# Performance work log

Hardware: AMD Instinct MI355X
Metric: run time of the kernel (lower is better)

The kernel has to match this reference:

```python
import jax, jax.numpy as jnp
import numpy as np

B, T, D, H, L = 32, 1024, 512, 512, 2
OUT = 512 * 2  # output_size is doubled in setup() (bidirectional)


def setup_inputs() -> dict:
    key = jax.random.key(0)
    ks = jax.random.split(key, 9)
    s = 1.0 / np.sqrt(H)
    return {
        "x": jax.random.normal(ks[0], (B, T, D), jnp.float32),
        "h0": jnp.zeros((L, B, H), jnp.float32),
        "c0": jnp.zeros((L, B, H), jnp.float32),
        # stacked LSTM weights, gate order (i, f, g, o) as in flax LSTMCell
        "Wi_f": jax.random.normal(ks[1], (L, D, 4 * H), jnp.float32) * s,
        "Wh_f": jax.random.normal(ks[2], (L, H, 4 * H), jnp.float32) * s,
        "b_f": jnp.zeros((L, 4 * H), jnp.float32),
        "Wi_b": jax.random.normal(ks[3], (L, D, 4 * H), jnp.float32) * s,
        "Wh_b": jax.random.normal(ks[4], (L, H, 4 * H), jnp.float32) * s,
        "b_b": jnp.zeros((L, 4 * H), jnp.float32),
        "W_out": jax.random.normal(ks[5], (2 * H, OUT), jnp.float32) * s,
        "b_out": jnp.zeros((OUT,), jnp.float32),
    }


def _lstm_layer(xs, h0, c0, Wi, Wh, b):
    # xs: [T, B, Din]; scans the sequential recurrence
    def step(carry, x_t):
        h, c = carry
        gates = x_t @ Wi + h @ Wh + b  # [B, 4H]
        i, f, g, o = jnp.split(gates, 4, axis=-1)
        c = jax.nn.sigmoid(f) * c + jax.nn.sigmoid(i) * jnp.tanh(g)
        h = jax.nn.sigmoid(o) * jnp.tanh(c)
        return (h, c), h

    _, hs = jax.lax.scan(step, (h0, c0), xs)
    return hs  # [T, B, H]


def _stack(xs, h0, c0, Wi, Wh, b):
    h = xs
    for l in range(Wi.shape[0]):  # small fixed layer loop
        h = _lstm_layer(h, h0[l], c0[l], Wi[l], Wh[l], b[l])
    return h


def reference(x, h0, c0, Wi_f, Wh_f, b_f, Wi_b, Wh_b, b_b, W_out, b_out):
    xs = jnp.swapaxes(x, 0, 1)  # [T, B, D]
    hf = _stack(xs, h0, c0, Wi_f, Wh_f, b_f)                # forward in time
    hb = _stack(xs[::-1], h0, c0, Wi_b, Wh_b, b_b)[::-1]    # backward in time
    out = jax.nn.relu(jnp.concatenate([hf, hb], axis=-1)) @ W_out + b_out
    return jnp.swapaxes(out, 0, 1)  # [B, T, 2*output_size]
```

## Files before the change

### kernel.cpp

```cpp
#include <hip/hip_runtime.h>
#include <math.h>

typedef __bf16 bf16;
typedef __bf16 bf16x8 __attribute__((ext_vector_type(8)));
typedef float f32x4 __attribute__((ext_vector_type(4)));
typedef int i32x4 __attribute__((ext_vector_type(4)));
typedef unsigned int u32;

#define TT 1024
#define BB 32
#define DD 512
#define HH 512
#define NG4 2048

#define OFF_FLAGS 0ull
#define FLAG_INTS (4u*1024u*64u)
#define OFF_ABORT ((size_t)FLAG_INTS*4ull)
#define OFF_WBT   (OFF_ABORT + 1024ull)
#define OFF_PL    (OFF_WBT + 2097152ull)
#define PL_BYTES  32768ull
#define OFF_H1    (OFF_PL + 4ull*2ull*16ull*PL_BYTES)
#define FULL_ELEM ((size_t)(TT+1)*BB*HH)

#define PLP(gg, pp, slot) (ws + OFF_PL + (((size_t)((gg)*2+(pp))*16 + (size_t)(slot))*PL_BYTES))

__device__ __forceinline__ bf16x8 load16_sc(const void* p) {
  i32x4 r;
  asm volatile("global_load_dwordx4 %0, %1, off sc0 sc1" : "=v"(r) : "v"(p) : "memory");
  return __builtin_bit_cast(bf16x8, r);
}
__device__ __forceinline__ void store_short_sc(void* p, u32 v) {
  asm volatile("global_store_short %0, %1, off sc0 sc1" :: "v"(p), "v"(v) : "memory");
}

__device__ __forceinline__ bool pollrow(int* row, int lane, int* abortf) {
  int it = 0;
  while (true) {
    int v = __hip_atomic_load(row + lane, __ATOMIC_RELAXED, __HIP_MEMORY_SCOPE_AGENT);
    if (__all(v != 0)) return true;
    __builtin_amdgcn_s_sleep(1);
    if ((++it & 1023) == 0) {
      if (it > (1 << 21)) {
        __hip_atomic_store(abortf, 1, __ATOMIC_RELAXED, __HIP_MEMORY_SCOPE_AGENT);
        return false;
      }
      if (__hip_atomic_load(abortf, __ATOMIC_RELAXED, __HIP_MEMORY_SCOPE_AGENT)) return false;
    }
  }
}

__global__ void k_setup(const float* __restrict__ h0,
                        const float* __restrict__ wout,
                        unsigned char* __restrict__ ws) {
  bf16* wbt  = (bf16*)(ws + OFF_WBT);
  int* flags = (int*)(ws + OFF_FLAGS);
  const u32 wcnt = 1024u*1024u;
  const u32 pcnt = 4u*BB*HH;
  const u32 fcnt = FLAG_INTS + 1u;
  const u32 total = wcnt + pcnt + fcnt;
  for (u32 i = blockIdx.x*blockDim.x + threadIdx.x; i < total; i += gridDim.x*blockDim.x) {
    if (i < wcnt) {
      u32 j = i >> 10, k = i & 1023u;
      wbt[(size_t)j*1024u + k] = (bf16)wout[(size_t)k*1024u + j];
    } else if (i < wcnt + pcnt) {
      u32 t = i - wcnt;
      u32 g = t >> 14;
      u32 rem = t & 16383u;
      u32 l = g >> 1;
      float v = h0[(size_t)l*(BB*HH) + rem];
      bf16 hi = (bf16)v;
      bf16 lo = (bf16)(v - (float)hi);
      ((bf16*)PLP(g, 0, 15))[rem] = hi;
      ((bf16*)PLP(g, 1, 15))[rem] = lo;
    } else {
      flags[i - wcnt - pcnt] = 0;
    }
  }
}

__launch_bounds__(256, 1)
__global__ void k_rnn(const float* __restrict__ x,
                      const float* __restrict__ c0,
                      const float* __restrict__ Wi_f, const float* __restrict__ Wh_f, const float* __restrict__ b_f,
                      const float* __restrict__ Wi_b, const float* __restrict__ Wh_b, const float* __restrict__ b_b,
                      unsigned char* __restrict__ ws) {
  __shared__ float gb[4][32][33];
  __shared__ int sab;

  const int bid = blockIdx.x;
  const int g = bid & 3;
  const int w = bid >> 2;
  const int l = g >> 1, d = g & 1;
  const int tid = threadIdx.x;
  const int lane = tid & 63;
  const int q = tid >> 6;

  const float* Wi   = (d ? Wi_b : Wi_f) + (size_t)l*DD*NG4;
  const float* Wh   = (d ? Wh_b : Wh_f) + (size_t)l*HH*NG4;
  const float* bias = (d ? b_b : b_f) + (size_t)l*NG4;

  int* flags  = (int*)(ws + OFF_FLAGS);
  int* abortf = flags + FLAG_INTS;

  const int lrow = lane & 15;
  const int kr0  = (lane >> 4) * 8;

  bf16x8 BWi[4][2], BWh[4][2], BWlo[4][2];
#pragma unroll
  for (int j = 0; j < 4; ++j) {
    int k0 = (q*4 + j)*32 + kr0;
#pragma unroll
    for (int nt = 0; nt < 2; ++nt) {
      int cc = nt*16 + lrow;
      int unit = cc >> 2, gate = cc & 3;
      int Jcol = gate*512 + w*8 + unit;
      bf16x8 ai, ah, al;
#pragma unroll
      for (int e = 0; e < 8; ++e) {
        float wi = Wi[(size_t)(k0+e)*NG4 + Jcol];
        float wh = Wh[(size_t)(k0+e)*NG4 + Jcol];
        ai[e] = (bf16)wi;
        bf16 hh = (bf16)wh;
        ah[e] = hh;
        al[e] = (bf16)(wh - (float)hh);
      }
      BWi[j][nt] = ai; BWh[j][nt] = ah; BWlo[j][nt] = al;
    }
  }

  u32 aoff[4][2];
#pragma unroll
  for (int j = 0; j < 4; ++j)
#pragma unroll
    for (int mt = 0; mt < 2; ++mt)
      aoff[j][mt] = (u32)((((mt*16 + lrow)*512) + (q*4 + j)*32 + kr0) * 2);

  const int bthr = tid >> 3, uthr = tid & 7;
  const int hu = w*8 + uthr;
  float cst = c0[((size_t)l*BB + bthr)*HH + hu];
  const float bgi = bias[hu], bgf = bias[512+hu], bgg = bias[1024+hu], bgo = bias[1536+hu];

  if (tid == 0) sab = 0;
  __syncthreads();

  for (int s = 0; s < TT; ++s) {
    const int slot_w = s & 15;
    const int slot_r = (s + 15) & 15;

    if (l == 1) {
      if (q == 1) { if (!pollrow(flags + ((size_t)d*1024 + s)*64, lane, abortf)) sab = 1; }
      __syncthreads();
    }

    f32x4 acc[2][2];
#pragma unroll
    for (int mt = 0; mt < 2; ++mt)
#pragma unroll
      for (int nt = 0; nt < 2; ++nt) acc[mt][nt] = (f32x4){0.f,0.f,0.f,0.f};

    if (l == 0) {
      const int t_time = d ? (TT-1-s) : s;
      bf16x8 Ax[4][2];
#pragma unroll
      for (int j = 0; j < 4; ++j)
#pragma unroll
        for (int mt = 0; mt < 2; ++mt) {
          const float* px = x + ((size_t)(mt*16 + lrow)*TT + t_time)*DD + (q*4 + j)*32 + kr0;
          float4 a  = *(const float4*)px;
          float4 b4 = *(const float4*)(px + 4);
          bf16x8 v = { (bf16)a.x,(bf16)a.y,(bf16)a.z,(bf16)a.w,
                       (bf16)b4.x,(bf16)b4.y,(bf16)b4.z,(bf16)b4.w };
          Ax[j][mt] = v;
        }
      if (q == 0 && s > 0)   { if (!pollrow(flags + ((size_t)g*1024 + (s-1))*64, lane, abortf)) sab = 1; }
      if (q == 1 && s >= 16) { if (!pollrow(flags + ((size_t)(2+d)*1024 + (s-16))*64, lane, abortf)) sab = 1; }
#pragma unroll
      for (int j = 0; j < 4; ++j)
#pragma unroll
        for (int mt = 0; mt < 2; ++mt)
#pragma unroll
          for (int nt = 0; nt < 2; ++nt)
            acc[mt][nt] = __builtin_amdgcn_mfma_f32_16x16x32_bf16(Ax[j][mt], BWi[j][nt], acc[mt][nt], 0, 0, 0);
    } else {
      const unsigned char* xb = PLP(d, 0, slot_w);
      bf16x8 Ax[4][2];
#pragma unroll
      for (int j = 0; j < 4; ++j)
#pragma unroll
        for (int mt = 0; mt < 2; ++mt)
          Ax[j][mt] = load16_sc(xb + aoff[j][mt]);
      if (q == 0 && s > 0) { if (!pollrow(flags + ((size_t)g*1024 + (s-1))*64, lane, abortf)) sab = 1; }
      asm volatile("s_waitcnt vmcnt(0)" ::: "memory");
      __builtin_amdgcn_sched_barrier(0);
#pragma unroll
      for (int j = 0; j < 4; ++j)
#pragma unroll
        for (int mt = 0; mt < 2; ++mt)
#pragma unroll
          for (int nt = 0; nt < 2; ++nt)
            acc[mt][nt] = __builtin_amdgcn_mfma_f32_16x16x32_bf16(Ax[j][mt], BWi[j][nt], acc[mt][nt], 0, 0, 0);
    }
    __syncthreads();
    if (sab) return;

    const unsigned char* hb = PLP(g, 0, slot_r);
    const unsigned char* lb = PLP(g, 1, slot_r);
    bf16x8 Ahi[4][2], Alo[4][2];
#pragma unroll
    for (int j = 0; j < 4; ++j)
#pragma unroll
      for (int mt = 0; mt < 2; ++mt) {
        Ahi[j][mt] = load16_sc(hb + aoff[j][mt]);
        Alo[j][mt] = load16_sc(lb + aoff[j][mt]);
      }
    asm volatile("s_waitcnt vmcnt(0)" ::: "memory");
    __builtin_amdgcn_sched_barrier(0);
#pragma unroll
    for (int j = 0; j < 4; ++j) {
#pragma unroll
      for (int mt = 0; mt < 2; ++mt)
#pragma unroll
        for (int nt = 0; nt < 2; ++nt)
          acc[mt][nt] = __builtin_amdgcn_mfma_f32_16x16x32_bf16(Ahi[j][mt], BWh[j][nt], acc[mt][nt], 0, 0, 0);
#pragma unroll
      for (int mt = 0; mt < 2; ++mt)
#pragma unroll
        for (int nt = 0; nt < 2; ++nt)
          acc[mt][nt] = __builtin_amdgcn_mfma_f32_16x16x32_bf16(Alo[j][mt], BWh[j][nt], acc[mt][nt], 0, 0, 0);
#pragma unroll
      for (int mt = 0; mt < 2; ++mt)
#pragma unroll
        for (int nt = 0; nt < 2; ++nt)
          acc[mt][nt] = __builtin_amdgcn_mfma_f32_16x16x32_bf16(Ahi[j][mt], BWlo[j][nt], acc[mt][nt], 0, 0, 0);
    }

#pragma unroll
    for (int mt = 0; mt < 2; ++mt)
#pragma unroll
      for (int nt = 0; nt < 2; ++nt)
#pragma unroll
        for (int r = 0; r < 4; ++r)
          gb[q][mt*16 + (lane>>4)*4 + r][nt*16 + lrow] = acc[mt][nt][r];
    __syncthreads();

    float gi = bgi, gf = bgf, gg2 = bgg, go = bgo;
#pragma unroll
    for (int qq = 0; qq < 4; ++qq) {
      gi  += gb[qq][bthr][uthr*4 + 0];
      gf  += gb[qq][bthr][uthr*4 + 1];
      gg2 += gb[qq][bthr][uthr*4 + 2];
      go  += gb[qq][bthr][uthr*4 + 3];
    }
    float si = 1.f/(1.f + __expf(-gi));
    float sf = 1.f/(1.f + __expf(-gf));
    float so = 1.f/(1.f + __expf(-go));
    cst = sf*cst + si*tanhf(gg2);
    float h = so*tanhf(cst);

    bf16 hh = (bf16)h;
    bf16 hl = (bf16)(h - (float)hh);
    u32 off2 = (u32)((bthr*512 + hu) * 2);
    store_short_sc((void*)(PLP(g, 0, slot_w) + off2), (u32)__builtin_bit_cast(unsigned short, hh));
    store_short_sc((void*)(PLP(g, 1, slot_w) + off2), (u32)__builtin_bit_cast(unsigned short, hl));
    if (l == 1) {
      float* H1 = (float*)(ws + OFF_H1) + (size_t)d*FULL_ELEM;
      H1[((size_t)(s+1)*BB + bthr)*HH + hu] = h;
    }
    asm volatile("s_waitcnt vmcnt(0)" ::: "memory");
    __syncthreads();
    if (tid == 0)
      __hip_atomic_store(flags + ((size_t)g*1024 + s)*64 + w, 1,
                         __ATOMIC_RELAXED, __HIP_MEMORY_SCOPE_AGENT);
  }
}

#define SWZG(row, bc) ((u32)(row)*128u + ((u32)(bc) ^ ((((u32)(row))&7u)<<4)))

__launch_bounds__(256, 2)
__global__ void k_out(const unsigned char* __restrict__ ws,
                      const float* __restrict__ bout,
                      float* __restrict__ out) {
  __shared__ unsigned char As[64*128];
  __shared__ unsigned char Bs[128*128];
  const float* Hf = (const float*)(ws + OFF_H1);
  const float* Hb = Hf + FULL_ELEM;
  const bf16* wbt = (const bf16*)(ws + OFF_WBT);

  const int m0 = blockIdx.x * 64;
  const int j0 = blockIdx.y * 128;
  const int tid = threadIdx.x, lane = tid & 63, q = tid >> 6;
  const int b = m0 >> 10;
  const int t0 = m0 & 1023;

  f32x4 acc[2][4];
#pragma unroll
  for (int mi = 0; mi < 2; ++mi)
#pragma unroll
    for (int ni = 0; ni < 4; ++ni) acc[mi][ni] = (f32x4){0.f,0.f,0.f,0.f};

  for (int kb = 0; kb < 16; ++kb) {
#pragma unroll
    for (int it = 0; it < 2; ++it) {
      int row = tid >> 2;
      int chunk = (tid & 3) + it*4;
      int k0 = kb*64 + chunk*8;
      int t = t0 + row;
      const float* src = (k0 < 512)
        ? (Hf + ((size_t)(t+1)*BB + b)*HH + k0)
        : (Hb + ((size_t)(TT-t)*BB + b)*HH + (k0-512));
      float4 fa = *(const float4*)src;
      float4 fb = *(const float4*)(src + 4);
      bf16x8 v = { (bf16)fmaxf(fa.x,0.f),(bf16)fmaxf(fa.y,0.f),(bf16)fmaxf(fa.z,0.f),(bf16)fmaxf(fa.w,0.f),
                   (bf16)fmaxf(fb.x,0.f),(bf16)fmaxf(fb.y,0.f),(bf16)fmaxf(fb.z,0.f),(bf16)fmaxf(fb.w,0.f) };
      *(bf16x8*)(As + SWZG(row, chunk*16)) = v;
    }
#pragma unroll
    for (int it = 0; it < 4; ++it) {
      int j = (tid >> 3) + it*32;
      int chunk = tid & 7;
      int k0 = kb*64 + chunk*8;
      bf16x8 v = *(const bf16x8*)(wbt + (size_t)(j0+j)*1024 + k0);
      *(bf16x8*)(Bs + SWZG(j, chunk*16)) = v;
    }
    __syncthreads();
    const int mrow = (q & 1)*32;
    const int nc0 = (q >> 1)*64;
#pragma unroll
    for (int ks = 0; ks < 2; ++ks) {
      u32 koff = (u32)(ks*32 + (lane>>4)*8) * 2u;
      bf16x8 afr[2];
#pragma unroll
      for (int mi = 0; mi < 2; ++mi)
        afr[mi] = *(const bf16x8*)(As + SWZG(mrow + mi*16 + (lane&15), koff));
#pragma unroll
      for (int ni = 0; ni < 4; ++ni) {
        bf16x8 bfr = *(const bf16x8*)(Bs + SWZG(nc0 + ni*16 + (lane&15), koff));
#pragma unroll
        for (int mi = 0; mi < 2; ++mi)
          acc[mi][ni] = __builtin_amdgcn_mfma_f32_16x16x32_bf16(afr[mi], bfr, acc[mi][ni], 0, 0, 0);
      }
    }
    __syncthreads();
  }
#pragma unroll
  for (int ni = 0; ni < 4; ++ni) {
    int col = j0 + (q >> 1)*64 + ni*16 + (lane & 15);
    float bv = bout[col];
#pragma unroll
    for (int mi = 0; mi < 2; ++mi) {
#pragma unroll
      for (int r = 0; r < 4; ++r) {
        int m = m0 + (q & 1)*32 + mi*16 + (lane >> 4)*4 + r;
        out[(size_t)m*1024 + col] = acc[mi][ni][r] + bv;
      }
    }
  }
}

extern "C" void kernel_launch(void* const* d_in, const int* in_sizes, int n_in,
                              void* d_out, int out_size, void* d_ws, size_t ws_size,
                              hipStream_t stream) {
  const float* x    = (const float*)d_in[0];
  const float* h0   = (const float*)d_in[1];
  const float* c0   = (const float*)d_in[2];
  const float* Wi_f = (const float*)d_in[3];
  const float* Wh_f = (const float*)d_in[4];
  const float* b_f  = (const float*)d_in[5];
  const float* Wi_b = (const float*)d_in[6];
  const float* Wh_b = (const float*)d_in[7];
  const float* b_b  = (const float*)d_in[8];
  const float* Wo   = (const float*)d_in[9];
  const float* bo   = (const float*)d_in[10];
  unsigned char* ws = (unsigned char*)d_ws;
  float* out = (float*)d_out;

  hipLaunchKernelGGL(k_setup, dim3(256), dim3(256), 0, stream, h0, Wo, ws);

  void* args[] = { (void*)&x, (void*)&c0, (void*)&Wi_f, (void*)&Wh_f, (void*)&b_f,
                   (void*)&Wi_b, (void*)&Wh_b, (void*)&b_b, (void*)&ws };
  hipError_t e = hipLaunchCooperativeKernel((const void*)k_rnn, dim3(256), dim3(256),
                                            args, 0, stream);
  if (e != hipSuccess) {
    hipLaunchKernelGGL(k_rnn, dim3(256), dim3(256), 0, stream,
                       x, c0, Wi_f, Wh_f, b_f, Wi_b, Wh_b, b_b, ws);
  }

  hipLaunchKernelGGL(k_out, dim3(512, 8), dim3(256), 0, stream,
                     (const unsigned char*)ws, bo, out);
}
```

Before: 6.435 ms.

## Prepack LSTM weight fragments, interleave hi/lo hidden state, prefetch x, store bf16 H1

The setup kernel now pre-packs the Wi/Wh hi/lo bf16 MFMA fragments, so each persistent RNN block loads them with contiguous 16-byte reads instead of strided scalar fp32 loads. The hi and lo bf16 halves of the hidden state are interleaved into one 32-bit word, so one store and paired vector loads replace two separate planes. Layer 0 prefetches the next timestep's x into registers while the current step runs. Polling spins briefly before sleeping and adds an acquire load. Layer-1 outputs are stored as bf16, halving output-GEMM input traffic at a small precision cost, and per-step unpacking adds ALU work.

```diff
diff --git a/kernel.cpp b/kernel.cpp
--- a/kernel.cpp
+++ b/kernel.cpp
@@ -6,86 +6,113 @@
 typedef float f32x4 __attribute__((ext_vector_type(4)));
 typedef int i32x4 __attribute__((ext_vector_type(4)));
 typedef unsigned int u32;
+typedef unsigned short u16;
 
 #define TT 1024
 #define BB 32
-#define DD 512
 #define HH 512
-#define NG4 2048
 
 #define OFF_FLAGS 0ull
-#define FLAG_INTS (4u*1024u*64u)
-#define OFF_ABORT ((size_t)FLAG_INTS*4ull)
-#define OFF_WBT   (OFF_ABORT + 1024ull)
-#define OFF_PL    (OFF_WBT + 2097152ull)
-#define PL_BYTES  32768ull
-#define OFF_H1    (OFF_PL + 4ull*2ull*16ull*PL_BYTES)
-#define FULL_ELEM ((size_t)(TT+1)*BB*HH)
-
-#define PLP(gg, pp, slot) (ws + OFF_PL + (((size_t)((gg)*2+(pp))*16 + (size_t)(slot))*PL_BYTES))
-
-__device__ __forceinline__ bf16x8 load16_sc(const void* p) {
-  i32x4 r;
-  asm volatile("global_load_dwordx4 %0, %1, off sc0 sc1" : "=v"(r) : "v"(p) : "memory");
-  return __builtin_bit_cast(bf16x8, r);
+#define OFF_CTL   1048576ull
+#define OFF_WBT   (OFF_CTL + 1024ull)
+#define OFF_FRAG  (OFF_WBT + 2097152ull)
+#define FRAG_B    8388608ull
+#define OFF_PL    (OFF_FRAG + 3ull*FRAG_B)
+#define PL_SLOT   65536ull
+#define PL_GRP    (16ull*PL_SLOT)
+#define OFF_H1    (OFF_PL + 4ull*PL_GRP)
+#define H1_ELEM   ((size_t)(TT+1)*BB*HH)
+
+__global__ void k_setup(const float* __restrict__ h0, const float* __restrict__ wout,
+                        const float* __restrict__ Wi_f, const float* __restrict__ Wh_f,
+                        const float* __restrict__ Wi_b, const float* __restrict__ Wh_b,
+                        unsigned char* __restrict__ ws) {
+  const u32 N0 = 1048576;
+  const u32 N1 = 65536;
+  const u32 N3 = 2097152;
+  const u32 N4 = 2097152;
+  const u32 N5 = 262145;
+  const u32 total = N0 + N1 + N3 + N4 + N5;
+  for (u32 i = blockIdx.x*blockDim.x + threadIdx.x; i < total; i += gridDim.x*blockDim.x) {
+    if (i < N0) {
+      u32 jj = i >> 10, kk = i & 1023u;
+      ((bf16*)(ws + OFF_WBT))[(size_t)jj*1024 + kk] = (bf16)wout[(size_t)kk*1024 + jj];
+    } else if (i < N0 + N1) {
+      u32 t = i - N0;
+      u32 g = t >> 14, r = t & 16383u;
+      u32 b = r >> 9, u = r & 511u, l = g >> 1;
+      float v = h0[((size_t)l*BB + b)*HH + u];
+      bf16 hi = (bf16)v;
+      bf16 lo = (bf16)(v - (float)hi);
+      u32 word = (u32)__builtin_bit_cast(u16, hi) | ((u32)__builtin_bit_cast(u16, lo) << 16);
+      *(u32*)(ws + OFF_PL + (size_t)g*PL_GRP + 15ull*PL_SLOT + (size_t)r*4) = word;
+    } else if (i < N0 + N1 + N3 + N4) {
+      u32 t = i - N0 - N1;
+      int isWh = (t >= N3);
+      if (isWh) t -= N3;
+      u32 e2 = t & 3u, lane = (t>>2)&63u, nt = (t>>8)&1u, j = (t>>9)&3u;
+      u32 q = (t>>11)&3u, w2 = (t>>13)&63u, g = (t>>19)&3u;
+      u32 l = g >> 1, d = g & 1;
+      u32 lrow = lane & 15u, kr0 = (lane>>4)*8u;
+      u32 cc = nt*16 + lrow;
+      u32 unit = cc >> 2, gate = cc & 3u;
+      u32 J = gate*512 + w2*8 + unit;
+      u32 k = (q*4 + j)*32 + kr0 + e2*2;
+      const float* src = isWh ? ((d ? Wh_b : Wh_f) + (size_t)l*HH*2048)
+                              : ((d ? Wi_b : Wi_f) + (size_t)l*HH*2048);
+      float v0 = src[(size_t)k*2048 + J];
+      float v1 = src[(size_t)(k+1)*2048 + J];
+      size_t fo = ((((size_t)(g*64+w2)*4 + q)*4 + j)*2 + nt)*64 + lane;
+      size_t byte = fo*16 + e2*4;
+      if (!isWh) {
+        *(u32*)(ws + OFF_FRAG + byte) =
+          (u32)__builtin_bit_cast(u16,(bf16)v0) | ((u32)__builtin_bit_cast(u16,(bf16)v1) << 16);
+      } else {
+        bf16 h0b = (bf16)v0, h1b = (bf16)v1;
+        bf16 l0b = (bf16)(v0 - (float)h0b), l1b = (bf16)(v1 - (float)h1b);
+        *(u32*)(ws + OFF_FRAG + FRAG_B + byte) =
+          (u32)__builtin_bit_cast(u16,h0b) | ((u32)__builtin_bit_cast(u16,h1b) << 16);
+        *(u32*)(ws + OFF_FRAG + 2ull*FRAG_B + byte) =
+          (u32)__builtin_bit_cast(u16,l0b) | ((u32)__builtin_bit_cast(u16,l1b) << 16);
+      }
+    } else {
+      u32 t = i - (N0+N1+N3+N4);
+      if (t < 262144u) ((int*)(ws + OFF_FLAGS))[t] = 0;
+      else *(int*)(ws + OFF_CTL) = 0;
+    }
+  }
 }
-__device__ __forceinline__ void store_short_sc(void* p, u32 v) {
-  asm volatile("global_store_short %0, %1, off sc0 sc1" :: "v"(p), "v"(v) : "memory");
-}
-
-__device__ __forceinline__ bool pollrow(int* row, int lane, int* abortf) {
+
+#define LD16(dst, p) asm volatile("global_load_dwordx4 %0, %1, off sc0 sc1" : "=v"(dst) : "v"(p) : "memory")
+#define ST4(p, v)    asm volatile("global_store_dword %0, %1, off sc0 sc1" :: "v"(p), "v"(v) : "memory")
+#define WAIT0() do { asm volatile("s_waitcnt vmcnt(0)" ::: "memory"); __builtin_amdgcn_sched_barrier(0); } while (0)
+
+__device__ __forceinline__ bool pollrow64(int* row, int lane, int* abortf) {
   int it = 0;
   while (true) {
     int v = __hip_atomic_load(row + lane, __ATOMIC_RELAXED, __HIP_MEMORY_SCOPE_AGENT);
-    if (__all(v != 0)) return true;
-    __builtin_amdgcn_s_sleep(1);
-    if ((++it & 1023) == 0) {
-      if (it > (1 << 21)) {
+    if (__all(v != 0)) {
+      (void)__hip_atomic_load(row + lane, __ATOMIC_ACQUIRE, __HIP_MEMORY_SCOPE_AGENT);
+      return true;
+    }
+    ++it;
+    if (it > 32) __builtin_amdgcn_s_sleep(1);
+    if ((it & 255) == 0) {
+      if (__hip_atomic_load(abortf, __ATOMIC_RELAXED, __HIP_MEMORY_SCOPE_AGENT)) return false;
+      if (it > (1 << 20)) {
         __hip_atomic_store(abortf, 1, __ATOMIC_RELAXED, __HIP_MEMORY_SCOPE_AGENT);
         return false;
       }
-      if (__hip_atomic_load(abortf, __ATOMIC_RELAXED, __HIP_MEMORY_SCOPE_AGENT)) return false;
     }
   }
 }
 
-__global__ void k_setup(const float* __restrict__ h0,
-                        const float* __restrict__ wout,
-                        unsigned char* __restrict__ ws) {
-  bf16* wbt  = (bf16*)(ws + OFF_WBT);
-  int* flags = (int*)(ws + OFF_FLAGS);
-  const u32 wcnt = 1024u*1024u;
-  const u32 pcnt = 4u*BB*HH;
-  const u32 fcnt = FLAG_INTS + 1u;
-  const u32 total = wcnt + pcnt + fcnt;
-  for (u32 i = blockIdx.x*blockDim.x + threadIdx.x; i < total; i += gridDim.x*blockDim.x) {
-    if (i < wcnt) {
-      u32 j = i >> 10, k = i & 1023u;
-      wbt[(size_t)j*1024u + k] = (bf16)wout[(size_t)k*1024u + j];
-    } else if (i < wcnt + pcnt) {
-      u32 t = i - wcnt;
-      u32 g = t >> 14;
-      u32 rem = t & 16383u;
-      u32 l = g >> 1;
-      float v = h0[(size_t)l*(BB*HH) + rem];
-      bf16 hi = (bf16)v;
-      bf16 lo = (bf16)(v - (float)hi);
-      ((bf16*)PLP(g, 0, 15))[rem] = hi;
-      ((bf16*)PLP(g, 1, 15))[rem] = lo;
-    } else {
-      flags[i - wcnt - pcnt] = 0;
-    }
-  }
-}
-
 __launch_bounds__(256, 1)
-__global__ void k_rnn(const float* __restrict__ x,
-                      const float* __restrict__ c0,
-                      const float* __restrict__ Wi_f, const float* __restrict__ Wh_f, const float* __restrict__ b_f,
-                      const float* __restrict__ Wi_b, const float* __restrict__ Wh_b, const float* __restrict__ b_b,
+__global__ void k_rnn(const float* __restrict__ x, const float* __restrict__ c0,
+                      const float* __restrict__ b_f, const float* __restrict__ b_b,
                       unsigned char* __restrict__ ws) {
   __shared__ float gb[4][32][33];
-  __shared__ int sab;
+  __shared__ int sdead;
 
   const int bid = blockIdx.x;
   const int g = bid & 3;
@@ -94,61 +121,61 @@
   const int tid = threadIdx.x;
   const int lane = tid & 63;
   const int q = tid >> 6;
-
-  const float* Wi   = (d ? Wi_b : Wi_f) + (size_t)l*DD*NG4;
-  const float* Wh   = (d ? Wh_b : Wh_f) + (size_t)l*HH*NG4;
-  const float* bias = (d ? b_b : b_f) + (size_t)l*NG4;
-
-  int* flags  = (int*)(ws + OFF_FLAGS);
-  int* abortf = flags + FLAG_INTS;
-
   const int lrow = lane & 15;
-  const int kr0  = (lane >> 4) * 8;
+  const int kr0 = (lane >> 4) * 8;
+
+  int* abortf = (int*)(ws + OFF_CTL);
+  int* flagw  = (int*)(ws + OFF_FLAGS);
+
+  if (tid == 0) sdead = 0;
 
   bf16x8 BWi[4][2], BWh[4][2], BWlo[4][2];
 #pragma unroll
-  for (int j = 0; j < 4; ++j) {
-    int k0 = (q*4 + j)*32 + kr0;
+  for (int j = 0; j < 4; ++j)
 #pragma unroll
     for (int nt = 0; nt < 2; ++nt) {
-      int cc = nt*16 + lrow;
-      int unit = cc >> 2, gate = cc & 3;
-      int Jcol = gate*512 + w*8 + unit;
-      bf16x8 ai, ah, al;
-#pragma unroll
-      for (int e = 0; e < 8; ++e) {
-        float wi = Wi[(size_t)(k0+e)*NG4 + Jcol];
-        float wh = Wh[(size_t)(k0+e)*NG4 + Jcol];
-        ai[e] = (bf16)wi;
-        bf16 hh = (bf16)wh;
-        ah[e] = hh;
-        al[e] = (bf16)(wh - (float)hh);
-      }
-      BWi[j][nt] = ai; BWh[j][nt] = ah; BWlo[j][nt] = al;
-    }
-  }
-
-  u32 aoff[4][2];
-#pragma unroll
-  for (int j = 0; j < 4; ++j)
-#pragma unroll
-    for (int mt = 0; mt < 2; ++mt)
-      aoff[j][mt] = (u32)((((mt*16 + lrow)*512) + (q*4 + j)*32 + kr0) * 2);
+      size_t fo = (((((size_t)(g*64+w)*4 + q)*4 + j)*2 + nt)*64 + lane) * 16;
+      BWi[j][nt]  = *(const bf16x8*)(ws + OFF_FRAG + fo);
+      BWh[j][nt]  = *(const bf16x8*)(ws + OFF_FRAG + FRAG_B + fo);
+      BWlo[j][nt] = *(const bf16x8*)(ws + OFF_FRAG + 2ull*FRAG_B + fo);
+    }
 
   const int bthr = tid >> 3, uthr = tid & 7;
   const int hu = w*8 + uthr;
   float cst = c0[((size_t)l*BB + bthr)*HH + hu];
+  const float* bias = (d ? b_b : b_f) + (size_t)l*2048;
   const float bgi = bias[hu], bgf = bias[512+hu], bgg = bias[1024+hu], bgo = bias[1536+hu];
 
-  if (tid == 0) sab = 0;
+  unsigned char* plOwn = ws + OFF_PL + (size_t)g*PL_GRP;
+  const unsigned char* plIn = ws + OFF_PL + (size_t)d*PL_GRP;
+  bf16* H1p = (bf16*)(ws + OFF_H1) + (size_t)d*H1_ELEM;
+
+  u32 ao[4][2];
+#pragma unroll
+  for (int j = 0; j < 4; ++j)
+#pragma unroll
+    for (int mt = 0; mt < 2; ++mt)
+      ao[j][mt] = (u32)((((mt*16 + lrow)*512) + (q*4 + j)*32 + kr0) * 4);
+
   __syncthreads();
+
+  float4 xr[16];
+  if (l == 0) {
+    int t0i = d ? (TT-1) : 0;
+#pragma unroll
+    for (int f = 0; f < 8; ++f) {
+      int j = f >> 1, mt = f & 1;
+      const float* px = x + (((size_t)(mt*16+lrow))*TT + t0i)*512 + (q*4 + j)*32 + kr0;
+      xr[f*2]   = *(const float4*)px;
+      xr[f*2+1] = *(const float4*)(px + 4);
+    }
+  }
 
   for (int s = 0; s < TT; ++s) {
     const int slot_w = s & 15;
-    const int slot_r = (s + 15) & 15;
 
     if (l == 1) {
-      if (q == 1) { if (!pollrow(flags + ((size_t)d*1024 + s)*64, lane, abortf)) sab = 1; }
+      if (q == 1) { if (!pollrow64(flagw + (size_t)(d*1024 + s)*64, lane, abortf)) sdead = 1; }
       __syncthreads();
     }
 
@@ -159,80 +186,92 @@
       for (int nt = 0; nt < 2; ++nt) acc[mt][nt] = (f32x4){0.f,0.f,0.f,0.f};
 
     if (l == 0) {
-      const int t_time = d ? (TT-1-s) : s;
-      bf16x8 Ax[4][2];
+      if (q == 0 && s > 0)  { if (!pollrow64(flagw + (size_t)(g*1024 + s-1)*64, lane, abortf)) sdead = 1; }
+      if (q == 1 && s >= 16){ if (!pollrow64(flagw + (size_t)((2+d)*1024 + s-16)*64, lane, abortf)) sdead = 1; }
+#pragma unroll
+      for (int f = 0; f < 8; ++f) {
+        int j = f >> 1, mt = f & 1;
+        float4 a = xr[f*2], b4 = xr[f*2+1];
+        bf16x8 ax = { (bf16)a.x,(bf16)a.y,(bf16)a.z,(bf16)a.w,
+                      (bf16)b4.x,(bf16)b4.y,(bf16)b4.z,(bf16)b4.w };
+#pragma unroll
+        for (int nt = 0; nt < 2; ++nt)
+          acc[mt][nt] = __builtin_amdgcn_mfma_f32_16x16x32_bf16(ax, BWi[j][nt], acc[mt][nt], 0, 0, 0);
+      }
+      if (s + 1 < TT) {
+        int tn = d ? (TT-2-s) : (s+1);
+#pragma unroll
+        for (int f = 0; f < 8; ++f) {
+          int j = f >> 1, mt = f & 1;
+          const float* px = x + (((size_t)(mt*16+lrow))*TT + tn)*512 + (q*4 + j)*32 + kr0;
+          xr[f*2]   = *(const float4*)px;
+          xr[f*2+1] = *(const float4*)(px + 4);
+        }
+      }
+    } else {
+      const unsigned char* xs = plIn + (size_t)slot_w*PL_SLOT;
+      i32x4 xm[4][2][2];
 #pragma unroll
       for (int j = 0; j < 4; ++j)
 #pragma unroll
         for (int mt = 0; mt < 2; ++mt) {
-          const float* px = x + ((size_t)(mt*16 + lrow)*TT + t_time)*DD + (q*4 + j)*32 + kr0;
-          float4 a  = *(const float4*)px;
-          float4 b4 = *(const float4*)(px + 4);
-          bf16x8 v = { (bf16)a.x,(bf16)a.y,(bf16)a.z,(bf16)a.w,
-                       (bf16)b4.x,(bf16)b4.y,(bf16)b4.z,(bf16)b4.w };
-          Ax[j][mt] = v;
+          LD16(xm[j][mt][0], xs + ao[j][mt]);
+          LD16(xm[j][mt][1], xs + ao[j][mt] + 16);
         }
-      if (q == 0 && s > 0)   { if (!pollrow(flags + ((size_t)g*1024 + (s-1))*64, lane, abortf)) sab = 1; }
-      if (q == 1 && s >= 16) { if (!pollrow(flags + ((size_t)(2+d)*1024 + (s-16))*64, lane, abortf)) sab = 1; }
+      if (q == 0 && s > 0) { if (!pollrow64(flagw + (size_t)(g*1024 + s-1)*64, lane, abortf)) sdead = 1; }
+      WAIT0();
 #pragma unroll
       for (int j = 0; j < 4; ++j)
 #pragma unroll
-        for (int mt = 0; mt < 2; ++mt)
+        for (int mt = 0; mt < 2; ++mt) {
+          i32x4 w0 = xm[j][mt][0], w1 = xm[j][mt][1];
+          i32x4 hi4;
+          hi4[0] = (int)(((u32)w0[0] & 0xFFFFu) | ((u32)w0[1] << 16));
+          hi4[1] = (int)(((u32)w0[2] & 0xFFFFu) | ((u32)w0[3] << 16));
+          hi4[2] = (int)(((u32)w1[0] & 0xFFFFu) | ((u32)w1[1] << 16));
+          hi4[3] = (int)(((u32)w1[2] & 0xFFFFu) | ((u32)w1[3] << 16));
+          bf16x8 ax = __builtin_bit_cast(bf16x8, hi4);
 #pragma unroll
           for (int nt = 0; nt < 2; ++nt)
-            acc[mt][nt] = __builtin_amdgcn_mfma_f32_16x16x32_bf16(Ax[j][mt], BWi[j][nt], acc[mt][nt], 0, 0, 0);
-    } else {
-      const unsigned char* xb = PLP(d, 0, slot_w);
-      bf16x8 Ax[4][2];
-#pragma unroll
-      for (int j = 0; j < 4; ++j)
-#pragma unroll
-        for (int mt = 0; mt < 2; ++mt)
-          Ax[j][mt] = load16_sc(xb + aoff[j][mt]);
-      if (q == 0 && s > 0) { if (!pollrow(flags + ((size_t)g*1024 + (s-1))*64, lane, abortf)) sab = 1; }
-      asm volatile("s_waitcnt vmcnt(0)" ::: "memory");
-      __builtin_amdgcn_sched_barrier(0);
-#pragma unroll
-      for (int j = 0; j < 4; ++j)
-#pragma unroll
-        for (int mt = 0; mt < 2; ++mt)
-#pragma unroll
-          for (int nt = 0; nt < 2; ++nt)
-            acc[mt][nt] = __builtin_amdgcn_mfma_f32_16x16x32_bf16(Ax[j][mt], BWi[j][nt], acc[mt][nt], 0, 0, 0);
+            acc[mt][nt] = __builtin_amdgcn_mfma_f32_16x16x32_bf16(ax, BWi[j][nt], acc[mt][nt], 0, 0, 0);
+        }
     }
     __syncthreads();
-    if (sab) return;
-
-    const unsigned char* hb = PLP(g, 0, slot_r);
-    const unsigned char* lb = PLP(g, 1, slot_r);
-    bf16x8 Ahi[4][2], Alo[4][2];
+    if (sdead) return;
+
+    const unsigned char* hs = plOwn + (size_t)((s + 15) & 15)*PL_SLOT;
+    i32x4 hw[4][2][2];
 #pragma unroll
     for (int j = 0; j < 4; ++j)
 #pragma unroll
       for (int mt = 0; mt < 2; ++mt) {
-        Ahi[j][mt] = load16_sc(hb + aoff[j][mt]);
-        Alo[j][mt] = load16_sc(lb + aoff[j][mt]);
-      }
-    asm volatile("s_waitcnt vmcnt(0)" ::: "memory");
-    __builtin_amdgcn_sched_barrier(0);
-#pragma unroll
-    for (int j = 0; j < 4; ++j) {
-#pragma unroll
-      for (int mt = 0; mt < 2; ++mt)
-#pragma unroll
-        for (int nt = 0; nt < 2; ++nt)
-          acc[mt][nt] = __builtin_amdgcn_mfma_f32_16x16x32_bf16(Ahi[j][mt], BWh[j][nt], acc[mt][nt], 0, 0, 0);
-#pragma unroll
-      for (int mt = 0; mt < 2; ++mt)
-#pragma unroll
-        for (int nt = 0; nt < 2; ++nt)
-          acc[mt][nt] = __builtin_amdgcn_mfma_f32_16x16x32_bf16(Alo[j][mt], BWh[j][nt], acc[mt][nt], 0, 0, 0);
-#pragma unroll
-      for (int mt = 0; mt < 2; ++mt)
-#pragma unroll
-        for (int nt = 0; nt < 2; ++nt)
-          acc[mt][nt] = __builtin_amdgcn_mfma_f32_16x16x32_bf16(Ahi[j][mt], BWlo[j][nt], acc[mt][nt], 0, 0, 0);
-    }
+        LD16(hw[j][mt][0], hs + ao[j][mt]);
+        LD16(hw[j][mt][1], hs + ao[j][mt] + 16);
+      }
+    WAIT0();
+#pragma unroll
+    for (int j = 0; j < 4; ++j)
+#pragma unroll
+      for (int mt = 0; mt < 2; ++mt) {
+        i32x4 w0 = hw[j][mt][0], w1 = hw[j][mt][1];
+        i32x4 hi4, lo4;
+        hi4[0] = (int)(((u32)w0[0] & 0xFFFFu) | ((u32)w0[1] << 16));
+        hi4[1] = (int)(((u32)w0[2] & 0xFFFFu) | ((u32)w0[3] << 16));
+        hi4[2] = (int)(((u32)w1[0] & 0xFFFFu) | ((u32)w1[1] << 16));
+        hi4[3] = (int)(((u32)w1[2] & 0xFFFFu) | ((u32)w1[3] << 16));
+        lo4[0] = (int)(((u32)w0[0] >> 16) | ((u32)w0[1] & 0xFFFF0000u));
+        lo4[1] = (int)(((u32)w0[2] >> 16) | ((u32)w0[3] & 0xFFFF0000u));
+        lo4[2] = (int)(((u32)w1[0] >> 16) | ((u32)w1[1] & 0xFFFF0000u));
+        lo4[3] = (int)(((u32)w1[2] >> 16) | ((u32)w1[3] & 0xFFFF0000u));
+        bf16x8 ahi = __builtin_bit_cast(bf16x8, hi4);
+        bf16x8 alo = __builtin_bit_cast(bf16x8, lo4);
+#pragma unroll
+        for (int nt = 0; nt < 2; ++nt) {
+          acc[mt][nt] = __builtin_amdgcn_mfma_f32_16x16x32_bf16(ahi, BWh[j][nt],  acc[mt][nt], 0, 0, 0);
+          acc[mt][nt] = __builtin_amdgcn_mfma_f32_16x16x32_bf16(alo, BWh[j][nt],  acc[mt][nt], 0, 0, 0);
+          acc[mt][nt] = __builtin_amdgcn_mfma_f32_16x16x32_bf16(ahi, BWlo[j][nt], acc[mt][nt], 0, 0, 0);
+        }
+      }
 
 #pragma unroll
     for (int mt = 0; mt < 2; ++mt)
@@ -257,19 +296,17 @@
     cst = sf*cst + si*tanhf(gg2);
     float h = so*tanhf(cst);
 
-    bf16 hh = (bf16)h;
-    bf16 hl = (bf16)(h - (float)hh);
-    u32 off2 = (u32)((bthr*512 + hu) * 2);
-    store_short_sc((void*)(PLP(g, 0, slot_w) + off2), (u32)__builtin_bit_cast(unsigned short, hh));
-    store_short_sc((void*)(PLP(g, 1, slot_w) + off2), (u32)__builtin_bit_cast(unsigned short, hl));
-    if (l == 1) {
-      float* H1 = (float*)(ws + OFF_H1) + (size_t)d*FULL_ELEM;
-      H1[((size_t)(s+1)*BB + bthr)*HH + hu] = h;
-    }
-    asm volatile("s_waitcnt vmcnt(0)" ::: "memory");
+    bf16 hhv = (bf16)h;
+    bf16 hlv = (bf16)(h - (float)hhv);
+    u32 word = (u32)__builtin_bit_cast(u16, hhv) | ((u32)__builtin_bit_cast(u16, hlv) << 16);
+    ST4(plOwn + (size_t)slot_w*PL_SLOT + (size_t)(bthr*512 + hu)*4, word);
+    if (l == 1)
+      H1p[((size_t)(s+1)*BB + bthr)*HH + hu] = hhv;
+
+    WAIT0();
     __syncthreads();
     if (tid == 0)
-      __hip_atomic_store(flags + ((size_t)g*1024 + s)*64 + w, 1,
+      __hip_atomic_store(flagw + (size_t)(g*1024 + s)*64 + w, 1,
                          __ATOMIC_RELAXED, __HIP_MEMORY_SCOPE_AGENT);
   }
 }
@@ -282,8 +319,8 @@
                       float* __restrict__ out) {
   __shared__ unsigned char As[64*128];
   __shared__ unsigned char Bs[128*128];
-  const float* Hf = (const float*)(ws + OFF_H1);
-  const float* Hb = Hf + FULL_ELEM;
+  const bf16* Hf = (const bf16*)(ws + OFF_H1);
+  const bf16* Hb = Hf + H1_ELEM;
   const bf16* wbt = (const bf16*)(ws + OFF_WBT);
 
   const int m0 = blockIdx.x * 64;
@@ -305,13 +342,12 @@
       int chunk = (tid & 3) + it*4;
       int k0 = kb*64 + chunk*8;
       int t = t0 + row;
-      const float* src = (k0 < 512)
+      const bf16* src = (k0 < 512)
         ? (Hf + ((size_t)(t+1)*BB + b)*HH + k0)
-        : (Hb + ((size_t)(TT-t)*BB + b)*HH + (k0-512));
-      float4 fa = *(const float4*)src;
-      float4 fb = *(const float4*)(src + 4);
-      bf16x8 v = { (bf16)fmaxf(fa.x,0.f),(bf16)fmaxf(fa.y,0.f),(bf16)fmaxf(fa.z,0.f),(bf16)fmaxf(fa.w,0.f),
-                   (bf16)fmaxf(fb.x,0.f),(bf16)fmaxf(fb.y,0.f),(bf16)fmaxf(fb.z,0.f),(bf16)fmaxf(fb.w,0.f) };
+        : (Hb + ((size_t)(TT - t)*BB + b)*HH + (k0 - 512));
+      bf16x8 v = *(const bf16x8*)src;
+#pragma unroll
+      for (int e = 0; e < 8; ++e) { if ((float)v[e] < 0.f) v[e] = (bf16)0.f; }
       *(bf16x8*)(As + SWZG(row, chunk*16)) = v;
     }
 #pragma unroll
@@ -374,15 +410,14 @@
   unsigned char* ws = (unsigned char*)d_ws;
   float* out = (float*)d_out;
 
-  hipLaunchKernelGGL(k_setup, dim3(256), dim3(256), 0, stream, h0, Wo, ws);
-
-  void* args[] = { (void*)&x, (void*)&c0, (void*)&Wi_f, (void*)&Wh_f, (void*)&b_f,
-                   (void*)&Wi_b, (void*)&Wh_b, (void*)&b_b, (void*)&ws };
+  hipLaunchKernelGGL(k_setup, dim3(2048), dim3(256), 0, stream,
+                     h0, Wo, Wi_f, Wh_f, Wi_b, Wh_b, ws);
+
+  void* args[] = { (void*)&x, (void*)&c0, (void*)&b_f, (void*)&b_b, (void*)&ws };
   hipError_t e = hipLaunchCooperativeKernel((const void*)k_rnn, dim3(256), dim3(256),
                                             args, 0, stream);
   if (e != hipSuccess) {
-    hipLaunchKernelGGL(k_rnn, dim3(256), dim3(256), 0, stream,
-                       x, c0, Wi_f, Wh_f, b_f, Wi_b, Wh_b, b_b, ws);
+    hipLaunchKernelGGL(k_rnn, dim3(256), dim3(256), 0, stream, x, c0, b_f, b_b, ws);
   }
 
   hipLaunchKernelGGL(k_out, dim3(512, 8), dim3(256), 0, stream,
```

Result: slower. 10.35 ms (+60.9%).
